# Kernel optimization log

Measured on AMD Instinct MI355X. Metric: run time of the kernel, lower is better.

## Reference

```python
import jax, jax.numpy as jnp
import numpy as np

B, I, H, O, T = 512, 512, 1024, 512, 128

def setup_inputs() -> dict:
    key = jax.random.key(0)
    ks = jax.random.split(key, 8)
    s_in = 1.0 / np.sqrt(I)
    s_h = 1.0 / np.sqrt(H)
    return {
        "x": jax.random.normal(ks[0], (B, I), dtype=jnp.float32),
        "h0": jnp.zeros((B, H), dtype=jnp.float32),
        "Wjx": jax.random.normal(ks[1], (H, I), dtype=jnp.float32) * s_in,
        "bjx": jnp.zeros((H,), dtype=jnp.float32),
        "Wjh": jax.random.normal(ks[2], (H, H), dtype=jnp.float32) * s_h,
        "bjh": jnp.zeros((H,), dtype=jnp.float32),
        "Wkx": jax.random.normal(ks[3], (H, I), dtype=jnp.float32) * s_in,
        "bkx": jnp.zeros((H,), dtype=jnp.float32),
        "Wkh": jax.random.normal(ks[4], (H, H), dtype=jnp.float32) * s_h,
        "bkh": jnp.zeros((H,), dtype=jnp.float32),
        "Wo": jax.random.normal(ks[5], (O, H), dtype=jnp.float32) * s_h,
        "bo": jnp.zeros((O,), dtype=jnp.float32),
        "seq_length": T,
    }

def reference(x, h0, Wjx, bjx, Wjh, bjh, Wkx, bkx, Wkh, bkh, Wo, bo, seq_length):
    # x is broadcast to every timestep (original repeats x along time).
    # Precompute the time-invariant input projections once; same math.
    jx = x @ Wjx.T + bjx  # [B,H]
    kx = x @ Wkx.T + bkx  # [B,H]

    def step(h, _):
        j = jax.nn.sigmoid(jx + h @ Wjh.T + bjh)
        k = jax.nn.sigmoid(kx + h @ Wkh.T + bkh)
        new_h = j * (1.0 - h) + (1.0 - k) * h
        out = new_h @ Wo.T + bo  # [B,O]
        return new_h, out

    h_final, outs = jax.lax.scan(step, h0, None, length=seq_length)
    outputs = jnp.transpose(outs, (1, 0, 2))  # [B,T,O]
    return outputs, h_final
```

## Files before the change

kernel.cpp:

```cpp
#include <hip/hip_runtime.h>
#include <hip/hip_bf16.h>
#include <hip/hip_cooperative_groups.h>

namespace cg = cooperative_groups;

constexpr int B = 512;
constexpr int I = 512;
constexpr int H = 1024;
constexpr int O = 512;

using short8 = __attribute__((ext_vector_type(8))) short;
using f32x4  = __attribute__((ext_vector_type(4))) float;
using bf16_t = __hip_bfloat16;

__device__ __forceinline__ short8 ldfrag(const bf16_t* p) {
    return *reinterpret_cast<const short8*>(p);
}
__device__ __forceinline__ float sigmoid_f(float z) {
    return 1.0f / (1.0f + __expf(-z));
}

__device__ __forceinline__ void group_wait(int* c, int target) {
    if (threadIdx.x == 0) {
        while (__hip_atomic_load(c, __ATOMIC_RELAXED, __HIP_MEMORY_SCOPE_AGENT) < target)
            __builtin_amdgcn_s_sleep(2);
    }
    __syncthreads();
    asm volatile("buffer_inv" ::: "memory");
}
__device__ __forceinline__ void group_post(int* c) {
    __syncthreads();
    if (threadIdx.x == 0)
        __hip_atomic_fetch_add(c, 1, __ATOMIC_RELAXED, __HIP_MEMORY_SCOPE_AGENT);
}

__global__ __launch_bounds__(256, 2)
void flipflop_rnn_kernel(const float* __restrict__ x,  const float* __restrict__ h0,
                         const float* __restrict__ Wjx, const float* __restrict__ bjx,
                         const float* __restrict__ Wjh, const float* __restrict__ bjh,
                         const float* __restrict__ Wkx, const float* __restrict__ bkx,
                         const float* __restrict__ Wkh, const float* __restrict__ bkh,
                         const float* __restrict__ Wo,  const float* __restrict__ bo,
                         const int* __restrict__ seqlen,
                         float* __restrict__ out,
                         bf16_t* __restrict__ wjh_bf, bf16_t* __restrict__ wkh_bf,
                         bf16_t* __restrict__ wo_bf,  bf16_t* __restrict__ wjx_bf,
                         bf16_t* __restrict__ wkx_bf, bf16_t* __restrict__ x_bf,
                         bf16_t* __restrict__ hbf0,   bf16_t* __restrict__ hbf1,
                         int* __restrict__ cnt)
{
    __shared__ short lds_w[32768];

    const int T    = seqlen[0];
    const int tid  = threadIdx.x;
    const int g    = blockIdx.x;
    const int nthr = gridDim.x * blockDim.x;
    const int gtid = g * blockDim.x + tid;

    for (int idx = gtid; idx < H * H; idx += nthr) wjh_bf[idx] = __float2bfloat16(Wjh[idx]);
    for (int idx = gtid; idx < H * H; idx += nthr) wkh_bf[idx] = __float2bfloat16(Wkh[idx]);
    for (int idx = gtid; idx < O * H; idx += nthr) wo_bf[idx]  = __float2bfloat16(Wo[idx]);
    for (int idx = gtid; idx < H * I; idx += nthr) wjx_bf[idx] = __float2bfloat16(Wjx[idx]);
    for (int idx = gtid; idx < H * I; idx += nthr) wkx_bf[idx] = __float2bfloat16(Wkx[idx]);
    for (int idx = gtid; idx < B * I; idx += nthr) x_bf[idx]   = __float2bfloat16(x[idx]);
    if (gtid < 8 * 256) cnt[gtid] = 0;

    const int w     = tid >> 6;
    const int lane  = tid & 63;
    const int quad  = lane >> 4;
    const int lm    = lane & 15;
    const int iblk  = g & 7;
    const int lblk  = g >> 3;
    const int rbase = iblk * 64 + w * 16;
    const int n0    = lblk * 16;
    const bool has_out = (lblk < 32);
    const int no0   = lblk * 16;
    int* grp_cnt = cnt + iblk * 256;

    float hreg[4];
    #pragma unroll
    for (int r = 0; r < 4; ++r) {
        const int row = rbase + quad * 4 + r;
        const int col = n0 + lm;
        const float hv = h0[row * H + col];
        hreg[r] = hv;
        hbf0[row * H + col] = __float2bfloat16(hv);
    }

    cg::this_grid().sync();

    for (int c = tid; c < 4096; c += 256) {
        const int gate = c >> 11;
        const int cc   = c & 2047;
        const int kb   = cc >> 4;
        const int col  = cc & 15;
        const bf16_t* src = (gate ? wkh_bf : wjh_bf) + (n0 + col) * H + kb * 8;
        *reinterpret_cast<short8*>(&lds_w[c * 8]) = *reinterpret_cast<const short8*>(src);
    }
    __syncthreads();

    float jxr[4], kxr[4];
    {
        f32x4 aJ = {0.f, 0.f, 0.f, 0.f};
        f32x4 aK = {0.f, 0.f, 0.f, 0.f};
        const bf16_t* aP = x_bf   + (rbase + lm) * I + quad * 8;
        const bf16_t* jP = wjx_bf + (n0 + lm) * I + quad * 8;
        const bf16_t* kP = wkx_bf + (n0 + lm) * I + quad * 8;
        #pragma unroll 4
        for (int k0 = 0; k0 < I; k0 += 32) {
            short8 a = ldfrag(aP + k0);
            aJ = __builtin_amdgcn_mfma_f32_16x16x32_bf16(a, ldfrag(jP + k0), aJ, 0, 0, 0);
            aK = __builtin_amdgcn_mfma_f32_16x16x32_bf16(a, ldfrag(kP + k0), aK, 0, 0, 0);
        }
        const int col = n0 + lm;
        #pragma unroll
        for (int r = 0; r < 4; ++r) {
            jxr[r] = aJ[r] + bjx[col] + bjh[col];
            kxr[r] = aK[r] + bkx[col] + bkh[col];
        }
    }
    const float bo_v = has_out ? bo[no0 + lm] : 0.0f;

    for (int t = 0; t < T; ++t) {
        if (t > 0) group_wait(grp_cnt + t, 64);
        const bf16_t* hb  = (t & 1) ? hbf1 : hbf0;
        bf16_t*       hbn = (t & 1) ? hbf0 : hbf1;

        f32x4 accJ = {0.f, 0.f, 0.f, 0.f};
        f32x4 accK = {0.f, 0.f, 0.f, 0.f};
        f32x4 accO = {0.f, 0.f, 0.f, 0.f};

        const bf16_t* aP = hb    + (rbase + lm) * H + quad * 8;
        const bf16_t* oP = wo_bf + (no0 + lm) * H + quad * 8;
        const short*  jL = lds_w + quad * 128 + lm * 8;
        const short*  kL = jL + 16384;

        if (has_out) {
            #pragma unroll 4
            for (int k0 = 0; k0 < H; k0 += 32) {
                short8 a  = ldfrag(aP + k0);
                short8 bj = *reinterpret_cast<const short8*>(jL + (k0 >> 3) * 128);
                short8 bk = *reinterpret_cast<const short8*>(kL + (k0 >> 3) * 128);
                accJ = __builtin_amdgcn_mfma_f32_16x16x32_bf16(a, bj, accJ, 0, 0, 0);
                accK = __builtin_amdgcn_mfma_f32_16x16x32_bf16(a, bk, accK, 0, 0, 0);
                accO = __builtin_amdgcn_mfma_f32_16x16x32_bf16(a, ldfrag(oP + k0), accO, 0, 0, 0);
            }
        } else {
            #pragma unroll 4
            for (int k0 = 0; k0 < H; k0 += 32) {
                short8 a  = ldfrag(aP + k0);
                short8 bj = *reinterpret_cast<const short8*>(jL + (k0 >> 3) * 128);
                short8 bk = *reinterpret_cast<const short8*>(kL + (k0 >> 3) * 128);
                accJ = __builtin_amdgcn_mfma_f32_16x16x32_bf16(a, bj, accJ, 0, 0, 0);
                accK = __builtin_amdgcn_mfma_f32_16x16x32_bf16(a, bk, accK, 0, 0, 0);
            }
        }

        if (has_out && t > 0) {
            #pragma unroll
            for (int r = 0; r < 4; ++r) {
                const int row = rbase + quad * 4 + r;
                out[(row * T + (t - 1)) * O + no0 + lm] = accO[r] + bo_v;
            }
        }

        #pragma unroll
        for (int r = 0; r < 4; ++r) {
            const int row = rbase + quad * 4 + r;
            const int col = n0 + lm;
            const float jv = sigmoid_f(accJ[r] + jxr[r]);
            const float kv = sigmoid_f(accK[r] + kxr[r]);
            const float hv = hreg[r];
            const float hn = jv * (1.0f - hv) + (1.0f - kv) * hv;
            hreg[r] = hn;
            hbn[row * H + col] = __float2bfloat16(hn);
        }

        group_post(grp_cnt + t + 1);
    }

    group_wait(grp_cnt + T, 64);

    {
        const bf16_t* hb = (T & 1) ? hbf1 : hbf0;
        if (has_out) {
            f32x4 accO = {0.f, 0.f, 0.f, 0.f};
            const bf16_t* aP = hb    + (rbase + lm) * H + quad * 8;
            const bf16_t* oP = wo_bf + (no0 + lm) * H + quad * 8;
            #pragma unroll 4
            for (int k0 = 0; k0 < H; k0 += 32) {
                accO = __builtin_amdgcn_mfma_f32_16x16x32_bf16(ldfrag(aP + k0), ldfrag(oP + k0), accO, 0, 0, 0);
            }
            #pragma unroll
            for (int r = 0; r < 4; ++r) {
                const int row = rbase + quad * 4 + r;
                out[(row * T + (T - 1)) * O + no0 + lm] = accO[r] + bo_v;
            }
        }
        const int hfin = B * T * O;
        #pragma unroll
        for (int r = 0; r < 4; ++r) {
            const int row = rbase + quad * 4 + r;
            const int col = n0 + lm;
            out[hfin + row * H + col] = hreg[r];
        }
    }
}

extern "C" void kernel_launch(void* const* d_in, const int* in_sizes, int n_in,
                              void* d_out, int out_size, void* d_ws, size_t ws_size,
                              hipStream_t stream) {
    const float* x   = (const float*)d_in[0];
    const float* h0  = (const float*)d_in[1];
    const float* Wjx = (const float*)d_in[2];
    const float* bjx = (const float*)d_in[3];
    const float* Wjh = (const float*)d_in[4];
    const float* bjh = (const float*)d_in[5];
    const float* Wkx = (const float*)d_in[6];
    const float* bkx = (const float*)d_in[7];
    const float* Wkh = (const float*)d_in[8];
    const float* bkh = (const float*)d_in[9];
    const float* Wo  = (const float*)d_in[10];
    const float* bo  = (const float*)d_in[11];
    const int* seqlen = (const int*)d_in[12];
    float* out = (float*)d_out;

    char* ws = (char*)d_ws;
    bf16_t* wjh_bf = (bf16_t*)(ws + 0);
    bf16_t* wkh_bf = (bf16_t*)(ws + 2097152);
    bf16_t* wo_bf  = (bf16_t*)(ws + 4194304);
    bf16_t* wjx_bf = (bf16_t*)(ws + 5242880);
    bf16_t* wkx_bf = (bf16_t*)(ws + 6291456);
    bf16_t* x_bf   = (bf16_t*)(ws + 7340032);
    bf16_t* hbf0   = (bf16_t*)(ws + 7864320);
    bf16_t* hbf1   = (bf16_t*)(ws + 8912896);
    int*    cnt    = (int*)   (ws + 9961472);

    void* args[] = {
        &x, &h0, &Wjx, &bjx, &Wjh, &bjh, &Wkx, &bkx, &Wkh, &bkh, &Wo, &bo,
        &seqlen, &out,
        &wjh_bf, &wkh_bf, &wo_bf, &wjx_bf, &wkx_bf, &x_bf, &hbf0, &hbf1, &cnt
    };
    hipLaunchCooperativeKernel((const void*)flipflop_rnn_kernel,
                               dim3(512), dim3(256), args, 0, stream);
}
```

Baseline: 2.026 ms.

## Widen per-block hidden tile to 32 columns and halve grid to 256 blocks

Each block now computes 32 hidden columns instead of 16, holding both column tiles of the Wjh/Wkh slices in a 128KB LDS buffer. The grid drops from 512 to 256 blocks, one per CU, and each group barrier waits for 32 posts instead of 64. Every h-fragment load from global memory now feeds six MFMAs instead of three, which cuts redundant reads of the hidden state and makes the per-step barrier smaller. In exchange each block does twice the serial work per step, and only one block runs per CU, which lowers occupancy and latency hiding.

Result: faster. 1.923 ms (-5.1%).

```diff
diff --git a/kernel.cpp b/kernel.cpp
--- a/kernel.cpp
+++ b/kernel.cpp
@@ -34,7 +34,7 @@
         __hip_atomic_fetch_add(c, 1, __ATOMIC_RELAXED, __HIP_MEMORY_SCOPE_AGENT);
 }
 
-__global__ __launch_bounds__(256, 2)
+__global__ __launch_bounds__(256, 1)
 void flipflop_rnn_kernel(const float* __restrict__ x,  const float* __restrict__ h0,
                          const float* __restrict__ Wjx, const float* __restrict__ bjx,
                          const float* __restrict__ Wjh, const float* __restrict__ bjh,
@@ -49,7 +49,7 @@
                          bf16_t* __restrict__ hbf0,   bf16_t* __restrict__ hbf1,
                          int* __restrict__ cnt)
 {
-    __shared__ short lds_w[32768];
+    __shared__ short lds_w[65536];
 
     const int T    = seqlen[0];
     const int tid  = threadIdx.x;
@@ -72,87 +72,111 @@
     const int iblk  = g & 7;
     const int lblk  = g >> 3;
     const int rbase = iblk * 64 + w * 16;
-    const int n0    = lblk * 16;
-    const bool has_out = (lblk < 32);
-    const int no0   = lblk * 16;
+    const int n0    = lblk * 32;
+    const bool has_out = (lblk < 16);
+    const int no0   = lblk * 32;
     int* grp_cnt = cnt + iblk * 256;
 
-    float hreg[4];
+    float hreg[2][4];
     #pragma unroll
-    for (int r = 0; r < 4; ++r) {
-        const int row = rbase + quad * 4 + r;
-        const int col = n0 + lm;
-        const float hv = h0[row * H + col];
-        hreg[r] = hv;
-        hbf0[row * H + col] = __float2bfloat16(hv);
+    for (int ct = 0; ct < 2; ++ct) {
+        #pragma unroll
+        for (int r = 0; r < 4; ++r) {
+            const int row = rbase + quad * 4 + r;
+            const int col = n0 + ct * 16 + lm;
+            const float hv = h0[row * H + col];
+            hreg[ct][r] = hv;
+            hbf0[row * H + col] = __float2bfloat16(hv);
+        }
     }
 
     cg::this_grid().sync();
 
-    for (int c = tid; c < 4096; c += 256) {
-        const int gate = c >> 11;
-        const int cc   = c & 2047;
-        const int kb   = cc >> 4;
-        const int col  = cc & 15;
+    for (int c = tid; c < 8192; c += 256) {
+        const int gate = c >> 12;
+        const int cc   = c & 4095;
+        const int kb   = cc >> 5;
+        const int col  = cc & 31;
         const bf16_t* src = (gate ? wkh_bf : wjh_bf) + (n0 + col) * H + kb * 8;
         *reinterpret_cast<short8*>(&lds_w[c * 8]) = *reinterpret_cast<const short8*>(src);
     }
     __syncthreads();
 
-    float jxr[4], kxr[4];
+    float jxr[2][4], kxr[2][4];
     {
-        f32x4 aJ = {0.f, 0.f, 0.f, 0.f};
-        f32x4 aK = {0.f, 0.f, 0.f, 0.f};
-        const bf16_t* aP = x_bf   + (rbase + lm) * I + quad * 8;
-        const bf16_t* jP = wjx_bf + (n0 + lm) * I + quad * 8;
-        const bf16_t* kP = wkx_bf + (n0 + lm) * I + quad * 8;
+        f32x4 aJ0 = {0.f,0.f,0.f,0.f}, aJ1 = {0.f,0.f,0.f,0.f};
+        f32x4 aK0 = {0.f,0.f,0.f,0.f}, aK1 = {0.f,0.f,0.f,0.f};
+        const bf16_t* aP  = x_bf   + (rbase + lm) * I + quad * 8;
+        const bf16_t* jP0 = wjx_bf + (n0 + lm) * I + quad * 8;
+        const bf16_t* jP1 = jP0 + 16 * I;
+        const bf16_t* kP0 = wkx_bf + (n0 + lm) * I + quad * 8;
+        const bf16_t* kP1 = kP0 + 16 * I;
         #pragma unroll 4
         for (int k0 = 0; k0 < I; k0 += 32) {
             short8 a = ldfrag(aP + k0);
-            aJ = __builtin_amdgcn_mfma_f32_16x16x32_bf16(a, ldfrag(jP + k0), aJ, 0, 0, 0);
-            aK = __builtin_amdgcn_mfma_f32_16x16x32_bf16(a, ldfrag(kP + k0), aK, 0, 0, 0);
-        }
-        const int col = n0 + lm;
-        #pragma unroll
-        for (int r = 0; r < 4; ++r) {
-            jxr[r] = aJ[r] + bjx[col] + bjh[col];
-            kxr[r] = aK[r] + bkx[col] + bkh[col];
-        }
-    }
-    const float bo_v = has_out ? bo[no0 + lm] : 0.0f;
+            aJ0 = __builtin_amdgcn_mfma_f32_16x16x32_bf16(a, ldfrag(jP0 + k0), aJ0, 0, 0, 0);
+            aJ1 = __builtin_amdgcn_mfma_f32_16x16x32_bf16(a, ldfrag(jP1 + k0), aJ1, 0, 0, 0);
+            aK0 = __builtin_amdgcn_mfma_f32_16x16x32_bf16(a, ldfrag(kP0 + k0), aK0, 0, 0, 0);
+            aK1 = __builtin_amdgcn_mfma_f32_16x16x32_bf16(a, ldfrag(kP1 + k0), aK1, 0, 0, 0);
+        }
+        #pragma unroll
+        for (int r = 0; r < 4; ++r) {
+            const int c0 = n0 + lm, c1 = n0 + 16 + lm;
+            jxr[0][r] = aJ0[r] + bjx[c0] + bjh[c0];
+            jxr[1][r] = aJ1[r] + bjx[c1] + bjh[c1];
+            kxr[0][r] = aK0[r] + bkx[c0] + bkh[c0];
+            kxr[1][r] = aK1[r] + bkx[c1] + bkh[c1];
+        }
+    }
+    const float bo_v0 = has_out ? bo[no0 + lm]      : 0.0f;
+    const float bo_v1 = has_out ? bo[no0 + 16 + lm] : 0.0f;
 
     for (int t = 0; t < T; ++t) {
-        if (t > 0) group_wait(grp_cnt + t, 64);
+        if (t > 0) group_wait(grp_cnt + t, 32);
         const bf16_t* hb  = (t & 1) ? hbf1 : hbf0;
         bf16_t*       hbn = (t & 1) ? hbf0 : hbf1;
 
-        f32x4 accJ = {0.f, 0.f, 0.f, 0.f};
-        f32x4 accK = {0.f, 0.f, 0.f, 0.f};
-        f32x4 accO = {0.f, 0.f, 0.f, 0.f};
-
-        const bf16_t* aP = hb    + (rbase + lm) * H + quad * 8;
-        const bf16_t* oP = wo_bf + (no0 + lm) * H + quad * 8;
-        const short*  jL = lds_w + quad * 128 + lm * 8;
-        const short*  kL = jL + 16384;
+        f32x4 accJ0 = {0.f,0.f,0.f,0.f}, accJ1 = {0.f,0.f,0.f,0.f};
+        f32x4 accK0 = {0.f,0.f,0.f,0.f}, accK1 = {0.f,0.f,0.f,0.f};
+        f32x4 accO0 = {0.f,0.f,0.f,0.f}, accO1 = {0.f,0.f,0.f,0.f};
+
+        const bf16_t* aP  = hb    + (rbase + lm) * H + quad * 8;
+        const bf16_t* oP0 = wo_bf + (no0 + lm) * H + quad * 8;
+        const bf16_t* oP1 = oP0 + 16 * H;
+        const short*  jL  = lds_w + quad * 256 + lm * 8;
+        const short*  kL  = jL + 32768;
 
         if (has_out) {
             #pragma unroll 4
             for (int k0 = 0; k0 < H; k0 += 32) {
-                short8 a  = ldfrag(aP + k0);
-                short8 bj = *reinterpret_cast<const short8*>(jL + (k0 >> 3) * 128);
-                short8 bk = *reinterpret_cast<const short8*>(kL + (k0 >> 3) * 128);
-                accJ = __builtin_amdgcn_mfma_f32_16x16x32_bf16(a, bj, accJ, 0, 0, 0);
-                accK = __builtin_amdgcn_mfma_f32_16x16x32_bf16(a, bk, accK, 0, 0, 0);
-                accO = __builtin_amdgcn_mfma_f32_16x16x32_bf16(a, ldfrag(oP + k0), accO, 0, 0, 0);
+                short8 a   = ldfrag(aP + k0);
+                const short* Lj = jL + (k0 >> 3) * 256;
+                const short* Lk = kL + (k0 >> 3) * 256;
+                short8 bj0 = *reinterpret_cast<const short8*>(Lj);
+                short8 bj1 = *reinterpret_cast<const short8*>(Lj + 128);
+                short8 bk0 = *reinterpret_cast<const short8*>(Lk);
+                short8 bk1 = *reinterpret_cast<const short8*>(Lk + 128);
+                accJ0 = __builtin_amdgcn_mfma_f32_16x16x32_bf16(a, bj0, accJ0, 0, 0, 0);
+                accJ1 = __builtin_amdgcn_mfma_f32_16x16x32_bf16(a, bj1, accJ1, 0, 0, 0);
+                accK0 = __builtin_amdgcn_mfma_f32_16x16x32_bf16(a, bk0, accK0, 0, 0, 0);
+                accK1 = __builtin_amdgcn_mfma_f32_16x16x32_bf16(a, bk1, accK1, 0, 0, 0);
+                accO0 = __builtin_amdgcn_mfma_f32_16x16x32_bf16(a, ldfrag(oP0 + k0), accO0, 0, 0, 0);
+                accO1 = __builtin_amdgcn_mfma_f32_16x16x32_bf16(a, ldfrag(oP1 + k0), accO1, 0, 0, 0);
             }
         } else {
             #pragma unroll 4
             for (int k0 = 0; k0 < H; k0 += 32) {
-                short8 a  = ldfrag(aP + k0);
-                short8 bj = *reinterpret_cast<const short8*>(jL + (k0 >> 3) * 128);
-                short8 bk = *reinterpret_cast<const short8*>(kL + (k0 >> 3) * 128);
-                accJ = __builtin_amdgcn_mfma_f32_16x16x32_bf16(a, bj, accJ, 0, 0, 0);
-                accK = __builtin_amdgcn_mfma_f32_16x16x32_bf16(a, bk, accK, 0, 0, 0);
+                short8 a   = ldfrag(aP + k0);
+                const short* Lj = jL + (k0 >> 3) * 256;
+                const short* Lk = kL + (k0 >> 3) * 256;
+                short8 bj0 = *reinterpret_cast<const short8*>(Lj);
+                short8 bj1 = *reinterpret_cast<const short8*>(Lj + 128);
+                short8 bk0 = *reinterpret_cast<const short8*>(Lk);
+                short8 bk1 = *reinterpret_cast<const short8*>(Lk + 128);
+                accJ0 = __builtin_amdgcn_mfma_f32_16x16x32_bf16(a, bj0, accJ0, 0, 0, 0);
+                accJ1 = __builtin_amdgcn_mfma_f32_16x16x32_bf16(a, bj1, accJ1, 0, 0, 0);
+                accK0 = __builtin_amdgcn_mfma_f32_16x16x32_bf16(a, bk0, accK0, 0, 0, 0);
+                accK1 = __builtin_amdgcn_mfma_f32_16x16x32_bf16(a, bk1, accK1, 0, 0, 0);
             }
         }
 
@@ -160,49 +184,63 @@
             #pragma unroll
             for (int r = 0; r < 4; ++r) {
                 const int row = rbase + quad * 4 + r;
-                out[(row * T + (t - 1)) * O + no0 + lm] = accO[r] + bo_v;
+                out[(row * T + (t - 1)) * O + no0 + lm]      = accO0[r] + bo_v0;
+                out[(row * T + (t - 1)) * O + no0 + 16 + lm] = accO1[r] + bo_v1;
             }
         }
 
         #pragma unroll
         for (int r = 0; r < 4; ++r) {
             const int row = rbase + quad * 4 + r;
-            const int col = n0 + lm;
-            const float jv = sigmoid_f(accJ[r] + jxr[r]);
-            const float kv = sigmoid_f(accK[r] + kxr[r]);
-            const float hv = hreg[r];
-            const float hn = jv * (1.0f - hv) + (1.0f - kv) * hv;
-            hreg[r] = hn;
-            hbn[row * H + col] = __float2bfloat16(hn);
+            {
+                const float jv = sigmoid_f(accJ0[r] + jxr[0][r]);
+                const float kv = sigmoid_f(accK0[r] + kxr[0][r]);
+                const float hv = hreg[0][r];
+                const float hn = jv * (1.0f - hv) + (1.0f - kv) * hv;
+                hreg[0][r] = hn;
+                hbn[row * H + n0 + lm] = __float2bfloat16(hn);
+            }
+            {
+                const float jv = sigmoid_f(accJ1[r] + jxr[1][r]);
+                const float kv = sigmoid_f(accK1[r] + kxr[1][r]);
+                const float hv = hreg[1][r];
+                const float hn = jv * (1.0f - hv) + (1.0f - kv) * hv;
+                hreg[1][r] = hn;
+                hbn[row * H + n0 + 16 + lm] = __float2bfloat16(hn);
+            }
         }
 
         group_post(grp_cnt + t + 1);
     }
 
-    group_wait(grp_cnt + T, 64);
+    group_wait(grp_cnt + T, 32);
 
     {
         const bf16_t* hb = (T & 1) ? hbf1 : hbf0;
         if (has_out) {
-            f32x4 accO = {0.f, 0.f, 0.f, 0.f};
-            const bf16_t* aP = hb    + (rbase + lm) * H + quad * 8;
-            const bf16_t* oP = wo_bf + (no0 + lm) * H + quad * 8;
+            f32x4 accO0 = {0.f,0.f,0.f,0.f}, accO1 = {0.f,0.f,0.f,0.f};
+            const bf16_t* aP  = hb    + (rbase + lm) * H + quad * 8;
+            const bf16_t* oP0 = wo_bf + (no0 + lm) * H + quad * 8;
+            const bf16_t* oP1 = oP0 + 16 * H;
             #pragma unroll 4
             for (int k0 = 0; k0 < H; k0 += 32) {
-                accO = __builtin_amdgcn_mfma_f32_16x16x32_bf16(ldfrag(aP + k0), ldfrag(oP + k0), accO, 0, 0, 0);
+                short8 a = ldfrag(aP + k0);
+                accO0 = __builtin_amdgcn_mfma_f32_16x16x32_bf16(a, ldfrag(oP0 + k0), accO0, 0, 0, 0);
+                accO1 = __builtin_amdgcn_mfma_f32_16x16x32_bf16(a, ldfrag(oP1 + k0), accO1, 0, 0, 0);
             }
             #pragma unroll
             for (int r = 0; r < 4; ++r) {
                 const int row = rbase + quad * 4 + r;
-                out[(row * T + (T - 1)) * O + no0 + lm] = accO[r] + bo_v;
+                out[(row * T + (T - 1)) * O + no0 + lm]      = accO0[r] + bo_v0;
+                out[(row * T + (T - 1)) * O + no0 + 16 + lm] = accO1[r] + bo_v1;
             }
         }
         const int hfin = B * T * O;
         #pragma unroll
         for (int r = 0; r < 4; ++r) {
             const int row = rbase + quad * 4 + r;
-            const int col = n0 + lm;
-            out[hfin + row * H + col] = hreg[r];
+            out[hfin + row * H + n0 + lm]      = hreg[0][r];
+            out[hfin + row * H + n0 + 16 + lm] = hreg[1][r];
         }
     }
 }
@@ -242,5 +280,5 @@
         &wjh_bf, &wkh_bf, &wo_bf, &wjx_bf, &wkx_bf, &x_bf, &hbf0, &hbf1, &cnt
     };
     hipLaunchCooperativeKernel((const void*)flipflop_rnn_kernel,
-                               dim3(512), dim3(256), args, 0, stream);
-}
+                               dim3(256), dim3(256), args, 0, stream);
+}
```
